# Optimization experiments

Measured on AMD Instinct MI355X. Metric: run time of the kernel, lower is better.

Reference implementation:

```python
import jax, jax.numpy as jnp
import numpy as np

EPS_BN = 1e-5
EPS_NORM = 1e-12
USER_NUM, ITEM_NUM = 100000, 50000
N_NODES = USER_NUM + ITEM_NUM
N_EDGES = 2400000
OUT_DIM, HID_DIM = 64, 128
BATCH = 4096


def setup_inputs() -> dict:
    key = jax.random.key(0)
    ks = jax.random.split(key, 12)
    f32 = jnp.float32
    return {
        "user_emb": jax.random.normal(ks[0], (USER_NUM, OUT_DIM), f32) * 0.1,
        "item_emb": jax.random.normal(ks[1], (ITEM_NUM, OUT_DIM), f32) * 0.1,
        "W0": jax.random.normal(ks[2], (OUT_DIM, HID_DIM), f32) * (1.0 / np.sqrt(OUT_DIM)),
        "b0": jnp.zeros((HID_DIM,), f32),
        "g0": jnp.ones((HID_DIM,), f32),
        "beta0": jnp.zeros((HID_DIM,), f32),
        "W1": jax.random.normal(ks[3], (HID_DIM, HID_DIM), f32) * (1.0 / np.sqrt(HID_DIM)),
        "b1": jnp.zeros((HID_DIM,), f32),
        "g1": jnp.ones((HID_DIM,), f32),
        "beta1": jnp.zeros((HID_DIM,), f32),
        "W2": jax.random.normal(ks[4], (HID_DIM, OUT_DIM), f32) * (1.0 / np.sqrt(HID_DIM)),
        "b2": jnp.zeros((OUT_DIM,), f32),
        "user_id": jax.random.randint(ks[5], (BATCH,), 0, USER_NUM),
        "pos_item": jax.random.randint(ks[6], (BATCH,), 0, ITEM_NUM),
        "neg_item": jax.random.randint(ks[7], (BATCH,), 0, ITEM_NUM),
        "edge_index": jax.random.randint(ks[8], (2, N_EDGES), 0, N_NODES),
    }


def _gcn_conv(x, W, b, src, dst, dis):
    # GCNConv with self-loops and symmetric normalization:
    # out_i = sum_{j->i} d_j^{-1/2} d_i^{-1/2} (x_j W) + d_i^{-1} (x_i W) + b
    h = x @ W                                   # [N, F]
    norm = dis[src] * dis[dst]                  # [E]
    msgs = h[src] * norm[:, None]               # [E, F] (irregular gather)
    agg = jax.ops.segment_sum(msgs, dst, num_segments=x.shape[0])
    self_loop = h * (dis * dis)[:, None]        # contribution of added self-loops
    return agg + self_loop + b


def _bn_train(x, gamma, beta):
    mean = jnp.mean(x, axis=0)
    var = jnp.mean((x - mean) ** 2, axis=0)     # biased var, as torch BN uses
    return (x - mean) * jax.lax.rsqrt(var + EPS_BN) * gamma + beta


def _l2norm(x):
    n = jnp.sqrt(jnp.sum(x * x, axis=-1, keepdims=True))
    return x / jnp.maximum(n, EPS_NORM)


def reference(user_emb, item_emb, W0, b0, g0, beta0, W1, b1, g1, beta1, W2, b2,
              user_id, pos_item, neg_item, edge_index):
    N = user_emb.shape[0] + item_emb.shape[0]
    src, dst = edge_index[0], edge_index[1]
    # degree includes self loop (weight 1 per edge + 1 self loop)
    deg = 1.0 + jax.ops.segment_sum(jnp.ones_like(src, user_emb.dtype), dst, num_segments=N)
    dis = jax.lax.rsqrt(deg)

    x = jnp.concatenate([user_emb, item_emb], axis=0)          # [N, OUT_DIM]

    # layer 0: conv -> BN -> ReLU -> (dropout: eval/identity) -> L2-normalize
    x = _l2norm(jax.nn.relu(_bn_train(_gcn_conv(x, W0, b0, src, dst, dis), g0, beta0)))
    # layer 1
    x = _l2norm(jax.nn.relu(_bn_train(_gcn_conv(x, W1, b1, src, dst, dis), g1, beta1)))
    # final conv
    x = _gcn_conv(x, W2, b2, src, dst, dis)                    # [N, OUT_DIM]

    user_embeddings = x[:user_emb.shape[0]]
    item_embeddings = x[user_emb.shape[0]:]
    u = user_embeddings[user_id]
    p = item_embeddings[pos_item]
    n = item_embeddings[neg_item]
    pos_score = jnp.sum(u * p, axis=-1)
    neg_score = jnp.sum(u * n, axis=-1)
    rec_loss = -jnp.mean(jax.nn.log_sigmoid(pos_score - neg_score))
    return rec_loss, x
```

## Files before the change

kernel.cpp:

```cpp
#include <hip/hip_runtime.h>
#include <hip/hip_bf16.h>
#include <math.h>

#define USER_NUM 100000
#define ITEM_NUM 50000
#define N_NODES  150000
#define N_EDGES  2400000
#define OUT_DIM  64
#define HID_DIM  128
#define BATCH    4096
#define EPS_BN   1e-5f

typedef unsigned short ushort_t;
typedef unsigned int uint_t;

__device__ __forceinline__ ushort_t f2bf(float f) {
    uint_t u = __float_as_uint(f);
    u += 0x7FFFu + ((u >> 16) & 1u);
    return (ushort_t)(u >> 16);
}
__device__ __forceinline__ float bf2f(ushort_t s) {
    return __uint_as_float((uint_t)s << 16);
}


__global__ __launch_bounds__(256) void zero_int_kernel(int* __restrict__ p, int n) {
    int i = blockIdx.x * 256 + threadIdx.x;
    if (i < n) p[i] = 0;
}

__global__ __launch_bounds__(256) void count_kernel(const int* __restrict__ dst, int* __restrict__ cnt) {
    int i = blockIdx.x * 256 + threadIdx.x;
    if (i < N_EDGES) atomicAdd(&cnt[dst[i]], 1);
}

__global__ __launch_bounds__(256) void dis_kernel(const int* __restrict__ cnt, float* __restrict__ dis) {
    int i = blockIdx.x * 256 + threadIdx.x;
    if (i < N_NODES) dis[i] = rsqrtf(1.0f + (float)cnt[i]);
}

#define SC_ELEM 1024
#define SC_NB   ((N_NODES + SC_ELEM - 1) / SC_ELEM)

__global__ __launch_bounds__(256) void scan_part_kernel(const int* __restrict__ cnt,
                                                        int* __restrict__ psum) {
    __shared__ int red[4];
    int tid = threadIdx.x;
    int base = blockIdx.x * SC_ELEM + tid * 4;
    int s = 0;
#pragma unroll
    for (int j = 0; j < 4; j++) { int i = base + j; if (i < N_NODES) s += cnt[i]; }
#pragma unroll
    for (int d = 1; d < 64; d <<= 1) s += __shfl_xor(s, d);
    if ((tid & 63) == 0) red[tid >> 6] = s;
    __syncthreads();
    if (tid == 0) psum[blockIdx.x] = red[0] + red[1] + red[2] + red[3];
}

__global__ __launch_bounds__(256) void scan_mid_kernel(int* __restrict__ psum,
                                                       int* __restrict__ off, int nb) {
    __shared__ int lds[256];
    int tid = threadIdx.x;
    int v = (tid < nb) ? psum[tid] : 0;
    lds[tid] = v;
    __syncthreads();
    for (int d = 1; d < 256; d <<= 1) {
        int t = (tid >= d) ? lds[tid - d] : 0;
        __syncthreads();
        lds[tid] += t;
        __syncthreads();
    }
    if (tid < nb) psum[tid] = lds[tid] - v;
    if (tid == 0) off[N_NODES] = lds[255];
}

__global__ __launch_bounds__(256) void scan_emit_kernel(const int* __restrict__ cnt,
                                                        const int* __restrict__ psum,
                                                        int* __restrict__ off) {
    __shared__ int lds[256];
    int tid = threadIdx.x;
    int base = blockIdx.x * SC_ELEM + tid * 4;
    int v[4]; int s = 0;
#pragma unroll
    for (int j = 0; j < 4; j++) {
        int i = base + j;
        v[j] = (i < N_NODES) ? cnt[i] : 0;
        s += v[j];
    }
    lds[tid] = s;
    __syncthreads();
    for (int d = 1; d < 256; d <<= 1) {
        int t = (tid >= d) ? lds[tid - d] : 0;
        __syncthreads();
        lds[tid] += t;
        __syncthreads();
    }
    int run = psum[blockIdx.x] + lds[tid] - s;
#pragma unroll
    for (int j = 0; j < 4; j++) {
        int i = base + j;
        if (i < N_NODES) off[i] = run;
        run += v[j];
    }
}


#define BSH   9
#define NBUCK ((N_NODES + 511) / 512)
#define P1_BLOCKS 512

__global__ __launch_bounds__(256) void bucket_part_kernel(const int* __restrict__ src,
                                                          const int* __restrict__ dst,
                                                          const int* __restrict__ off,
                                                          int* __restrict__ bcur,
                                                          uint2* __restrict__ temp) {
    __shared__ int hist[NBUCK];
    __shared__ int base[NBUCK];
    const int per = (N_EDGES + P1_BLOCKS - 1) / P1_BLOCKS;
    const int lo = blockIdx.x * per;
    int hi = lo + per; if (hi > N_EDGES) hi = N_EDGES;
    const int tid = threadIdx.x;
    for (int j = tid; j < NBUCK; j += 256) hist[j] = 0;
    __syncthreads();
    for (int i = lo + tid; i < hi; i += 256)
        atomicAdd(&hist[dst[i] >> BSH], 1);
    __syncthreads();
    for (int b = tid; b < NBUCK; b += 256) {
        int h = hist[b];
        if (h > 0) base[b] = off[b << BSH] + atomicAdd(&bcur[b], h);
    }
    __syncthreads();
    for (int i = lo + tid; i < hi; i += 256) {
        int d = dst[i];
        int p = atomicAdd(&base[d >> BSH], 1);
        temp[p] = make_uint2((uint_t)src[i], (uint_t)d);
    }
}

__global__ __launch_bounds__(256) void bucket_fine_kernel(const int* __restrict__ off,
                                                          const float* __restrict__ dis,
                                                          const uint2* __restrict__ temp,
                                                          uint2* __restrict__ csr8) {
    __shared__ int   offs[513];
    __shared__ int   cur[512];
    __shared__ float disd[512];
    const int b  = blockIdx.x;
    const int lo = b << BSH;
    int hi = lo + 512; if (hi > N_NODES) hi = N_NODES;
    const int nn = hi - lo;
    const int tid = threadIdx.x;
    for (int j = tid; j <= nn; j += 256) offs[j] = off[lo + j];
    for (int j = tid; j < nn; j += 256) { cur[j] = 0; disd[j] = dis[lo + j]; }
    __syncthreads();
    const int e0 = offs[0], e1 = offs[nn];
    for (int i = e0 + tid; i < e1; i += 256) {
        uint2 t = temp[i];
        int dl = (int)t.y - lo;
        int p = offs[dl] + atomicAdd(&cur[dl], 1);
        float wv = dis[t.x] * disd[dl];
        csr8[p] = make_uint2(t.x, __float_as_uint(wv));
    }
}


__device__ __forceinline__ float4 load4(const float* p) { return *(const float4*)p; }
__device__ __forceinline__ float4 load4(const ushort_t* p) {
    ushort4 u = *(const ushort4*)p;
    return make_float4(bf2f(u.x), bf2f(u.y), bf2f(u.z), bf2f(u.w));
}

template<typename XT, int DIN, int DOUT, int MBLK>
__global__ __launch_bounds__(256) void gemm_kernel(const XT* __restrict__ xlo,
                                                   const XT* __restrict__ xhi, int split,
                                                   const float* __restrict__ W,
                                                   ushort_t* __restrict__ out, int nrows) {
    constexpr int KC    = 32;
    constexpr int NC    = DIN / KC;
    constexpr int XS_PT = MBLK / 32;
    constexpr int WS_PT = DOUT / 32;
    constexpr int NCOLG = DOUT / 8;

    __shared__ float xs[MBLK][KC + 1];
    __shared__ float ws[KC][DOUT];

    const int tid  = threadIdx.x;
    const int row0 = blockIdx.x * MBLK;
    const int colg = tid % NCOLG;
    const int rowg = tid / NCOLG;

    float4 xr[XS_PT], wr[WS_PT];

    auto load_chunk = [&](int kc) {
#pragma unroll
        for (int i = 0; i < XS_PT; i++) {
            int idx = i * 256 + tid;
            int m = idx >> 3, kq = idx & 7;
            int row = row0 + m; if (row > nrows - 1) row = nrows - 1;
            const XT* rp = (row < split) ? xlo + (size_t)row * DIN
                                         : xhi + (size_t)(row - split) * DIN;
            xr[i] = load4(rp + kc + kq * 4);
        }
#pragma unroll
        for (int i = 0; i < WS_PT; i++) {
            int idx = i * 256 + tid;
            int n4 = idx % (DOUT / 4), kk = idx / (DOUT / 4);
            wr[i] = *(const float4*)(W + (size_t)(kc + kk) * DOUT + n4 * 4);
        }
    };
    auto write_chunk = [&]() {
#pragma unroll
        for (int i = 0; i < XS_PT; i++) {
            int idx = i * 256 + tid;
            int m = idx >> 3, kq = idx & 7;
            xs[m][kq * 4 + 0] = xr[i].x;
            xs[m][kq * 4 + 1] = xr[i].y;
            xs[m][kq * 4 + 2] = xr[i].z;
            xs[m][kq * 4 + 3] = xr[i].w;
        }
#pragma unroll
        for (int i = 0; i < WS_PT; i++) {
            int idx = i * 256 + tid;
            int n4 = idx % (DOUT / 4), kk = idx / (DOUT / 4);
            *(float4*)&ws[kk][n4 * 4] = wr[i];
        }
    };

    float acc[8][8];
#pragma unroll
    for (int r = 0; r < 8; r++)
#pragma unroll
        for (int c = 0; c < 8; c++) acc[r][c] = 0.f;

    load_chunk(0);
    write_chunk();
    __syncthreads();

    for (int c = 0; c < NC; c++) {
        if (c + 1 < NC) load_chunk((c + 1) * KC);
#pragma unroll 4
        for (int k = 0; k < KC; k++) {
            float4 wa = *(const float4*)&ws[k][colg * 8];
            float4 wb = *(const float4*)&ws[k][colg * 8 + 4];
            float xv[8];
#pragma unroll
            for (int r = 0; r < 8; r++) xv[r] = xs[rowg * 8 + r][k];
#pragma unroll
            for (int r = 0; r < 8; r++) {
                acc[r][0] = fmaf(xv[r], wa.x, acc[r][0]);
                acc[r][1] = fmaf(xv[r], wa.y, acc[r][1]);
                acc[r][2] = fmaf(xv[r], wa.z, acc[r][2]);
                acc[r][3] = fmaf(xv[r], wa.w, acc[r][3]);
                acc[r][4] = fmaf(xv[r], wb.x, acc[r][4]);
                acc[r][5] = fmaf(xv[r], wb.y, acc[r][5]);
                acc[r][6] = fmaf(xv[r], wb.z, acc[r][6]);
                acc[r][7] = fmaf(xv[r], wb.w, acc[r][7]);
            }
        }
        __syncthreads();
        if (c + 1 < NC) { write_chunk(); __syncthreads(); }
    }

#pragma unroll
    for (int r = 0; r < 8; r++) {
        int row = row0 + rowg * 8 + r;
        if (row < nrows) {
            uint4 pk;
            pk.x = (uint_t)f2bf(acc[r][0]) | ((uint_t)f2bf(acc[r][1]) << 16);
            pk.y = (uint_t)f2bf(acc[r][2]) | ((uint_t)f2bf(acc[r][3]) << 16);
            pk.z = (uint_t)f2bf(acc[r][4]) | ((uint_t)f2bf(acc[r][5]) << 16);
            pk.w = (uint_t)f2bf(acc[r][6]) | ((uint_t)f2bf(acc[r][7]) << 16);
            *(uint4*)&out[(size_t)row * DOUT + colg * 8] = pk;
        }
    }
}


template<int DOUT>
__global__ __launch_bounds__(256) void agg_kernel(const ushort_t* __restrict__ h,
                                                  const float* __restrict__ dis,
                                                  const int* __restrict__ off,
                                                  const uint2* __restrict__ csr8,
                                                  const float* __restrict__ bias,
                                                  float* __restrict__ out, int n) {
    int wave = threadIdx.x >> 6;
    int lane = threadIdx.x & 63;
    int node = blockIdx.x * 4 + wave;
    if (node >= n) return;
    float di  = dis[node];
    int   beg = off[node], end = off[node + 1];
    if (DOUT == 128) {
        const uint_t* hp = (const uint_t*)h;
        float ax = 0.f, ay = 0.f;
        int e = beg;
        for (; e + 4 <= end; e += 4) {
            uint2 e0 = csr8[e], e1 = csr8[e + 1], e2 = csr8[e + 2], e3 = csr8[e + 3];
            uint_t u0 = hp[(size_t)e0.x * 64 + lane];
            uint_t u1 = hp[(size_t)e1.x * 64 + lane];
            uint_t u2 = hp[(size_t)e2.x * 64 + lane];
            uint_t u3 = hp[(size_t)e3.x * 64 + lane];
            float w0 = __uint_as_float(e0.y), w1 = __uint_as_float(e1.y);
            float w2 = __uint_as_float(e2.y), w3 = __uint_as_float(e3.y);
            ax = fmaf(__uint_as_float(u0 << 16), w0, ax);
            ay = fmaf(__uint_as_float(u0 & 0xFFFF0000u), w0, ay);
            ax = fmaf(__uint_as_float(u1 << 16), w1, ax);
            ay = fmaf(__uint_as_float(u1 & 0xFFFF0000u), w1, ay);
            ax = fmaf(__uint_as_float(u2 << 16), w2, ax);
            ay = fmaf(__uint_as_float(u2 & 0xFFFF0000u), w2, ay);
            ax = fmaf(__uint_as_float(u3 << 16), w3, ax);
            ay = fmaf(__uint_as_float(u3 & 0xFFFF0000u), w3, ay);
        }
        for (; e < end; e++) {
            uint2 ev = csr8[e];
            float wv = __uint_as_float(ev.y);
            uint_t u = hp[(size_t)ev.x * 64 + lane];
            ax = fmaf(__uint_as_float(u << 16), wv, ax);
            ay = fmaf(__uint_as_float(u & 0xFFFF0000u), wv, ay);
        }
        uint_t us = hp[(size_t)node * 64 + lane];
        float2 bb = ((const float2*)bias)[lane];
        float dd = di * di;
        float2 o;
        o.x = ax + __uint_as_float(us << 16) * dd + bb.x;
        o.y = ay + __uint_as_float(us & 0xFFFF0000u) * dd + bb.y;
        ((float2*)out)[(size_t)node * 64 + lane] = o;
    } else {
        float ax = 0.f;
        int e = beg;
        for (; e + 4 <= end; e += 4) {
            uint2 e0 = csr8[e], e1 = csr8[e + 1], e2 = csr8[e + 2], e3 = csr8[e + 3];
            float h0 = bf2f(h[(size_t)e0.x * 64 + lane]);
            float h1 = bf2f(h[(size_t)e1.x * 64 + lane]);
            float h2 = bf2f(h[(size_t)e2.x * 64 + lane]);
            float h3 = bf2f(h[(size_t)e3.x * 64 + lane]);
            ax = fmaf(h0, __uint_as_float(e0.y), ax);
            ax = fmaf(h1, __uint_as_float(e1.y), ax);
            ax = fmaf(h2, __uint_as_float(e2.y), ax);
            ax = fmaf(h3, __uint_as_float(e3.y), ax);
        }
        for (; e < end; e++) {
            uint2 ev = csr8[e];
            ax = fmaf(bf2f(h[(size_t)ev.x * 64 + lane]), __uint_as_float(ev.y), ax);
        }
        float hs = bf2f(h[(size_t)node * 64 + lane]);
        out[(size_t)node * 64 + lane] = ax + hs * di * di + bias[lane];
    }
}


#define STATS_NB 512

__global__ __launch_bounds__(128) void stats1_kernel(const float* __restrict__ x,
                                                     double* __restrict__ part) {
    int col = threadIdx.x;
    double a = 0.0, b = 0.0;
    for (int row = blockIdx.x; row < N_NODES; row += STATS_NB) {
        float v = x[(size_t)row * HID_DIM + col];
        a += v;
        b += (double)v * (double)v;
    }
    part[(size_t)blockIdx.x * 256 + col]       = a;
    part[(size_t)blockIdx.x * 256 + 128 + col] = b;
}

__global__ __launch_bounds__(256) void stats2_kernel(const double* __restrict__ part,
                                                     const float* __restrict__ g,
                                                     const float* __restrict__ beta,
                                                     float* __restrict__ a_out,
                                                     float* __restrict__ b_out) {
    __shared__ double red1[4], red2[4];
    int col = blockIdx.x;
    int tid = threadIdx.x;
    double s1 = 0.0, s2 = 0.0;
    for (int p = tid; p < STATS_NB; p += 256) {
        s1 += part[(size_t)p * 256 + col];
        s2 += part[(size_t)p * 256 + 128 + col];
    }
#pragma unroll
    for (int d = 32; d >= 1; d >>= 1) {
        s1 += __shfl_xor(s1, d);
        s2 += __shfl_xor(s2, d);
    }
    int wave = tid >> 6, lane = tid & 63;
    if (lane == 0) { red1[wave] = s1; red2[wave] = s2; }
    __syncthreads();
    if (tid == 0) {
        double t1 = red1[0] + red1[1] + red1[2] + red1[3];
        double t2 = red2[0] + red2[1] + red2[2] + red2[3];
        double mean = t1 / (double)N_NODES;
        double var  = t2 / (double)N_NODES - mean * mean;
        float inv = rsqrtf((float)var + EPS_BN);
        float aa  = g[col] * inv;
        a_out[col] = aa;
        b_out[col] = beta[col] - (float)mean * aa;
    }
}


__global__ __launch_bounds__(256) void bn_relu_l2_kernel(const float* __restrict__ in,
                                                         const float* __restrict__ a,
                                                         const float* __restrict__ b,
                                                         uint_t* __restrict__ outp, int n) {
    int wave = threadIdx.x >> 6;
    int lane = threadIdx.x & 63;
    int row  = blockIdx.x * 4 + wave;
    if (row >= n) return;
    float2 v  = *(const float2*)(in + (size_t)row * 128 + lane * 2);
    float2 aa = *(const float2*)(a + lane * 2);
    float2 bb = *(const float2*)(b + lane * 2);
    float y0 = fmaxf(fmaf(v.x, aa.x, bb.x), 0.f);
    float y1 = fmaxf(fmaf(v.y, aa.y, bb.y), 0.f);
    float ss = y0 * y0 + y1 * y1;
#pragma unroll
    for (int d = 32; d >= 1; d >>= 1) ss += __shfl_xor(ss, d);
    float nn  = sqrtf(ss);
    float inv = 1.f / fmaxf(nn, 1e-12f);
    uint_t pk = (uint_t)f2bf(y0 * inv) | ((uint_t)f2bf(y1 * inv) << 16);
    outp[(size_t)row * 64 + lane] = pk;
}


__global__ void zero_float_kernel(float* p) { *p = 0.f; }

__global__ __launch_bounds__(256) void loss_kernel(const float* __restrict__ X,
                                                   const int* __restrict__ uid,
                                                   const int* __restrict__ pid,
                                                   const int* __restrict__ nid,
                                                   float* __restrict__ out0) {
    int wave = threadIdx.x >> 6;
    int lane = threadIdx.x & 63;
    int b = blockIdx.x * 4 + wave;
    if (b >= BATCH) return;
    const float* u = X + (size_t)uid[b] * OUT_DIM;
    const float* p = X + (size_t)(USER_NUM + pid[b]) * OUT_DIM;
    const float* q = X + (size_t)(USER_NUM + nid[b]) * OUT_DIM;
    float uv = u[lane];
    float ps = uv * p[lane];
    float ns = uv * q[lane];
#pragma unroll
    for (int d = 32; d >= 1; d >>= 1) {
        ps += __shfl_xor(ps, d);
        ns += __shfl_xor(ns, d);
    }
    if (lane == 0) {
        float t  = ns - ps;
        float sp = fmaxf(t, 0.f) + log1pf(expf(-fabsf(t)));
        atomicAdd(out0, sp * (1.0f / BATCH));
    }
}


extern "C" void kernel_launch(void* const* d_in, const int* in_sizes, int n_in,
                              void* d_out, int out_size, void* d_ws, size_t ws_size,
                              hipStream_t stream) {
    const float* user_emb = (const float*)d_in[0];
    const float* item_emb = (const float*)d_in[1];
    const float* W0  = (const float*)d_in[2];
    const float* b0  = (const float*)d_in[3];
    const float* g0  = (const float*)d_in[4];
    const float* be0 = (const float*)d_in[5];
    const float* W1  = (const float*)d_in[6];
    const float* b1  = (const float*)d_in[7];
    const float* g1  = (const float*)d_in[8];
    const float* be1 = (const float*)d_in[9];
    const float* W2  = (const float*)d_in[10];
    const float* b2  = (const float*)d_in[11];
    const int* user_id  = (const int*)d_in[12];
    const int* pos_item = (const int*)d_in[13];
    const int* neg_item = (const int*)d_in[14];
    const int* edge     = (const int*)d_in[15];
    const int* src = edge;
    const int* dst = edge + N_EDGES;

    char* w = (char*)d_ws;
    auto alloc = [&](size_t bytes) -> char* {
        char* r = w;
        w += (bytes + 255) / 256 * 256;
        return r;
    };
    int*      cnt  = (int*)alloc((size_t)N_NODES * 4);
    int*      off  = (int*)alloc((size_t)(N_NODES + 1) * 4);
    int*      bcur = (int*)alloc((size_t)NBUCK * 4);
    uint2*    csr8 = (uint2*)alloc((size_t)N_EDGES * 8);
    float*    dis  = (float*)alloc((size_t)N_NODES * 4);
    int*      psum = (int*)alloc((size_t)SC_NB * 4);
    double*   part = (double*)alloc((size_t)STATS_NB * 256 * 8);
    float*    bn_a = (float*)alloc(128 * 4);
    float*    bn_b = (float*)alloc(128 * 4);
    ushort_t* hbuf = (ushort_t*)alloc((size_t)N_NODES * HID_DIM * 2);
    float*    xbuf = (float*)alloc((size_t)N_NODES * HID_DIM * 4);
    ushort_t* xbf  = (ushort_t*)alloc((size_t)N_NODES * HID_DIM * 2);

    uint2* temp = (uint2*)hbuf;

    float* out = (float*)d_out;
    float* X   = out + 1;

    const int EB = (N_EDGES + 255) / 256;
    const int NB = (N_NODES + 255) / 256;
    const int AGGB = (N_NODES + 3) / 4;

    zero_int_kernel<<<NB, 256, 0, stream>>>(cnt, N_NODES);
    count_kernel<<<EB, 256, 0, stream>>>(dst, cnt);
    dis_kernel<<<NB, 256, 0, stream>>>(cnt, dis);
    scan_part_kernel<<<SC_NB, 256, 0, stream>>>(cnt, psum);
    scan_mid_kernel<<<1, 256, 0, stream>>>(psum, off, SC_NB);
    scan_emit_kernel<<<SC_NB, 256, 0, stream>>>(cnt, psum, off);
    zero_int_kernel<<<(NBUCK + 255) / 256, 256, 0, stream>>>(bcur, NBUCK);
    bucket_part_kernel<<<P1_BLOCKS, 256, 0, stream>>>(src, dst, off, bcur, temp);
    bucket_fine_kernel<<<NBUCK, 256, 0, stream>>>(off, dis, temp, csr8);

    gemm_kernel<float, 64, 128, 128><<<(N_NODES + 127) / 128, 256, 0, stream>>>(
        user_emb, item_emb, USER_NUM, W0, hbuf, N_NODES);
    agg_kernel<128><<<AGGB, 256, 0, stream>>>(hbuf, dis, off, csr8, b0, xbuf, N_NODES);
    stats1_kernel<<<STATS_NB, 128, 0, stream>>>(xbuf, part);
    stats2_kernel<<<128, 256, 0, stream>>>(part, g0, be0, bn_a, bn_b);
    bn_relu_l2_kernel<<<AGGB, 256, 0, stream>>>(xbuf, bn_a, bn_b, (uint_t*)xbf, N_NODES);

    gemm_kernel<ushort_t, 128, 128, 128><<<(N_NODES + 127) / 128, 256, 0, stream>>>(
        xbf, xbf, N_NODES, W1, hbuf, N_NODES);
    agg_kernel<128><<<AGGB, 256, 0, stream>>>(hbuf, dis, off, csr8, b1, xbuf, N_NODES);
    stats1_kernel<<<STATS_NB, 128, 0, stream>>>(xbuf, part);
    stats2_kernel<<<128, 256, 0, stream>>>(part, g1, be1, bn_a, bn_b);
    bn_relu_l2_kernel<<<AGGB, 256, 0, stream>>>(xbuf, bn_a, bn_b, (uint_t*)xbf, N_NODES);

    gemm_kernel<ushort_t, 128, 64, 256><<<(N_NODES + 255) / 256, 256, 0, stream>>>(
        xbf, xbf, N_NODES, W2, hbuf, N_NODES);
    agg_kernel<64><<<AGGB, 256, 0, stream>>>(hbuf, dis, off, csr8, b2, X, N_NODES);

    zero_float_kernel<<<1, 1, 0, stream>>>(out);
    loss_kernel<<<(BATCH + 3) / 4, 256, 0, stream>>>(X, user_id, pos_item, neg_item, out);
}
```

Measured before the change: 1.077 ms.

## Rewrite node-feature GEMM to use bf16 MFMA matrix instructions

Replaces the FP32 FMA shared-memory tiled GEMM with a kernel that uses 16x16x32 bf16 MFMA instructions. The weights are converted to bf16 and held transposed in LDS, and each wave computes 32 rows directly from global loads. This targets the dense projection cost in each GCN layer. In exchange, weights and the first-layer embeddings are rounded to bf16, and output stores become narrow 2-byte scattered writes.

Measured after the change: 967.5 us. 1.11x faster.

```diff
diff --git a/kernel.cpp b/kernel.cpp
--- a/kernel.cpp
+++ b/kernel.cpp
@@ -13,6 +13,9 @@
 
 typedef unsigned short ushort_t;
 typedef unsigned int uint_t;
+
+typedef __attribute__((ext_vector_type(8))) __bf16 bf16x8;
+typedef __attribute__((ext_vector_type(4))) float f32x4;
 
 __device__ __forceinline__ ushort_t f2bf(float f) {
     uint_t u = __float_as_uint(f);
@@ -163,113 +166,78 @@
 }
 
 
-__device__ __forceinline__ float4 load4(const float* p) { return *(const float4*)p; }
-__device__ __forceinline__ float4 load4(const ushort_t* p) {
-    ushort4 u = *(const ushort4*)p;
-    return make_float4(bf2f(u.x), bf2f(u.y), bf2f(u.z), bf2f(u.w));
-}
-
-template<typename XT, int DIN, int DOUT, int MBLK>
+__device__ __forceinline__ bf16x8 loadA(const ushort_t* p) {
+    uint4 u = *(const uint4*)p;
+    return __builtin_bit_cast(bf16x8, u);
+}
+__device__ __forceinline__ bf16x8 loadA(const float* p) {
+    float4 f0 = *(const float4*)p;
+    float4 f1 = *(const float4*)(p + 4);
+    uint4 u;
+    u.x = (uint_t)f2bf(f0.x) | ((uint_t)f2bf(f0.y) << 16);
+    u.y = (uint_t)f2bf(f0.z) | ((uint_t)f2bf(f0.w) << 16);
+    u.z = (uint_t)f2bf(f1.x) | ((uint_t)f2bf(f1.y) << 16);
+    u.w = (uint_t)f2bf(f1.z) | ((uint_t)f2bf(f1.w) << 16);
+    return __builtin_bit_cast(bf16x8, u);
+}
+
+template<typename XT, int DIN, int DOUT>
 __global__ __launch_bounds__(256) void gemm_kernel(const XT* __restrict__ xlo,
                                                    const XT* __restrict__ xhi, int split,
                                                    const float* __restrict__ W,
                                                    ushort_t* __restrict__ out, int nrows) {
-    constexpr int KC    = 32;
-    constexpr int NC    = DIN / KC;
-    constexpr int XS_PT = MBLK / 32;
-    constexpr int WS_PT = DOUT / 32;
-    constexpr int NCOLG = DOUT / 8;
-
-    __shared__ float xs[MBLK][KC + 1];
-    __shared__ float ws[KC][DOUT];
-
-    const int tid  = threadIdx.x;
-    const int row0 = blockIdx.x * MBLK;
-    const int colg = tid % NCOLG;
-    const int rowg = tid / NCOLG;
-
-    float4 xr[XS_PT], wr[WS_PT];
-
-    auto load_chunk = [&](int kc) {
-#pragma unroll
-        for (int i = 0; i < XS_PT; i++) {
-            int idx = i * 256 + tid;
-            int m = idx >> 3, kq = idx & 7;
-            int row = row0 + m; if (row > nrows - 1) row = nrows - 1;
-            const XT* rp = (row < split) ? xlo + (size_t)row * DIN
-                                         : xhi + (size_t)(row - split) * DIN;
-            xr[i] = load4(rp + kc + kq * 4);
+    constexpr int LDW = DIN + 8;
+    constexpr int NCT = DOUT / 16;
+    __shared__ ushort_t wt[DOUT][LDW];
+
+    const int tid = threadIdx.x;
+    for (int idx = tid; idx < DIN * DOUT; idx += 256) {
+        int k = idx / DOUT, n = idx % DOUT;
+        wt[n][k] = f2bf(W[idx]);
+    }
+    __syncthreads();
+
+    const int wave = tid >> 6, lane = tid & 63;
+    const int lm = lane & 15, lk = lane >> 4;
+    const int row0 = blockIdx.x * 128 + wave * 32;
+
+    f32x4 acc[2][NCT];
+#pragma unroll
+    for (int rt = 0; rt < 2; rt++)
+#pragma unroll
+        for (int c = 0; c < NCT; c++) acc[rt][c] = (f32x4){0.f, 0.f, 0.f, 0.f};
+
+    const XT* rp[2];
+#pragma unroll
+    for (int rt = 0; rt < 2; rt++) {
+        int row = row0 + rt * 16 + lm;
+        if (row > nrows - 1) row = nrows - 1;
+        rp[rt] = (row < split) ? xlo + (size_t)row * DIN
+                               : xhi + (size_t)(row - split) * DIN;
+    }
+
+#pragma unroll
+    for (int ks = 0; ks < DIN / 32; ks++) {
+        bf16x8 a0 = loadA(rp[0] + ks * 32 + lk * 8);
+        bf16x8 a1 = loadA(rp[1] + ks * 32 + lk * 8);
+#pragma unroll
+        for (int c = 0; c < NCT; c++) {
+            bf16x8 b = *(const bf16x8*)&wt[c * 16 + lm][ks * 32 + lk * 8];
+            acc[0][c] = __builtin_amdgcn_mfma_f32_16x16x32_bf16(a0, b, acc[0][c], 0, 0, 0);
+            acc[1][c] = __builtin_amdgcn_mfma_f32_16x16x32_bf16(a1, b, acc[1][c], 0, 0, 0);
         }
-#pragma unroll
-        for (int i = 0; i < WS_PT; i++) {
-            int idx = i * 256 + tid;
-            int n4 = idx % (DOUT / 4), kk = idx / (DOUT / 4);
-            wr[i] = *(const float4*)(W + (size_t)(kc + kk) * DOUT + n4 * 4);
-        }
-    };
-    auto write_chunk = [&]() {
-#pragma unroll
-        for (int i = 0; i < XS_PT; i++) {
-            int idx = i * 256 + tid;
-            int m = idx >> 3, kq = idx & 7;
-            xs[m][kq * 4 + 0] = xr[i].x;
-            xs[m][kq * 4 + 1] = xr[i].y;
-            xs[m][kq * 4 + 2] = xr[i].z;
-            xs[m][kq * 4 + 3] = xr[i].w;
-        }
-#pragma unroll
-        for (int i = 0; i < WS_PT; i++) {
-            int idx = i * 256 + tid;
-            int n4 = idx % (DOUT / 4), kk = idx / (DOUT / 4);
-            *(float4*)&ws[kk][n4 * 4] = wr[i];
-        }
-    };
-
-    float acc[8][8];
-#pragma unroll
-    for (int r = 0; r < 8; r++)
-#pragma unroll
-        for (int c = 0; c < 8; c++) acc[r][c] = 0.f;
-
-    load_chunk(0);
-    write_chunk();
-    __syncthreads();
-
-    for (int c = 0; c < NC; c++) {
-        if (c + 1 < NC) load_chunk((c + 1) * KC);
-#pragma unroll 4
-        for (int k = 0; k < KC; k++) {
-            float4 wa = *(const float4*)&ws[k][colg * 8];
-            float4 wb = *(const float4*)&ws[k][colg * 8 + 4];
-            float xv[8];
-#pragma unroll
-            for (int r = 0; r < 8; r++) xv[r] = xs[rowg * 8 + r][k];
-#pragma unroll
-            for (int r = 0; r < 8; r++) {
-                acc[r][0] = fmaf(xv[r], wa.x, acc[r][0]);
-                acc[r][1] = fmaf(xv[r], wa.y, acc[r][1]);
-                acc[r][2] = fmaf(xv[r], wa.z, acc[r][2]);
-                acc[r][3] = fmaf(xv[r], wa.w, acc[r][3]);
-                acc[r][4] = fmaf(xv[r], wb.x, acc[r][4]);
-                acc[r][5] = fmaf(xv[r], wb.y, acc[r][5]);
-                acc[r][6] = fmaf(xv[r], wb.z, acc[r][6]);
-                acc[r][7] = fmaf(xv[r], wb.w, acc[r][7]);
+    }
+
+#pragma unroll
+    for (int rt = 0; rt < 2; rt++) {
+#pragma unroll
+        for (int r = 0; r < 4; r++) {
+            int row = row0 + rt * 16 + lk * 4 + r;
+            if (row < nrows) {
+#pragma unroll
+                for (int c = 0; c < NCT; c++)
+                    out[(size_t)row * DOUT + c * 16 + lm] = f2bf(acc[rt][c][r]);
             }
-        }
-        __syncthreads();
-        if (c + 1 < NC) { write_chunk(); __syncthreads(); }
-    }
-
-#pragma unroll
-    for (int r = 0; r < 8; r++) {
-        int row = row0 + rowg * 8 + r;
-        if (row < nrows) {
-            uint4 pk;
-            pk.x = (uint_t)f2bf(acc[r][0]) | ((uint_t)f2bf(acc[r][1]) << 16);
-            pk.y = (uint_t)f2bf(acc[r][2]) | ((uint_t)f2bf(acc[r][3]) << 16);
-            pk.z = (uint_t)f2bf(acc[r][4]) | ((uint_t)f2bf(acc[r][5]) << 16);
-            pk.w = (uint_t)f2bf(acc[r][6]) | ((uint_t)f2bf(acc[r][7]) << 16);
-            *(uint4*)&out[(size_t)row * DOUT + colg * 8] = pk;
         }
     }
 }
@@ -498,6 +466,7 @@
     const int EB = (N_EDGES + 255) / 256;
     const int NB = (N_NODES + 255) / 256;
     const int AGGB = (N_NODES + 3) / 4;
+    const int GB = (N_NODES + 127) / 128;
 
     zero_int_kernel<<<NB, 256, 0, stream>>>(cnt, N_NODES);
     count_kernel<<<EB, 256, 0, stream>>>(dst, cnt);
@@ -509,21 +478,21 @@
     bucket_part_kernel<<<P1_BLOCKS, 256, 0, stream>>>(src, dst, off, bcur, temp);
     bucket_fine_kernel<<<NBUCK, 256, 0, stream>>>(off, dis, temp, csr8);
 
-    gemm_kernel<float, 64, 128, 128><<<(N_NODES + 127) / 128, 256, 0, stream>>>(
+    gemm_kernel<float, 64, 128><<<GB, 256, 0, stream>>>(
         user_emb, item_emb, USER_NUM, W0, hbuf, N_NODES);
     agg_kernel<128><<<AGGB, 256, 0, stream>>>(hbuf, dis, off, csr8, b0, xbuf, N_NODES);
     stats1_kernel<<<STATS_NB, 128, 0, stream>>>(xbuf, part);
     stats2_kernel<<<128, 256, 0, stream>>>(part, g0, be0, bn_a, bn_b);
     bn_relu_l2_kernel<<<AGGB, 256, 0, stream>>>(xbuf, bn_a, bn_b, (uint_t*)xbf, N_NODES);
 
-    gemm_kernel<ushort_t, 128, 128, 128><<<(N_NODES + 127) / 128, 256, 0, stream>>>(
+    gemm_kernel<ushort_t, 128, 128><<<GB, 256, 0, stream>>>(
         xbf, xbf, N_NODES, W1, hbuf, N_NODES);
     agg_kernel<128><<<AGGB, 256, 0, stream>>>(hbuf, dis, off, csr8, b1, xbuf, N_NODES);
     stats1_kernel<<<STATS_NB, 128, 0, stream>>>(xbuf, part);
     stats2_kernel<<<128, 256, 0, stream>>>(part, g1, be1, bn_a, bn_b);
     bn_relu_l2_kernel<<<AGGB, 256, 0, stream>>>(xbuf, bn_a, bn_b, (uint_t*)xbf, N_NODES);
 
-    gemm_kernel<ushort_t, 128, 64, 256><<<(N_NODES + 255) / 256, 256, 0, stream>>>(
+    gemm_kernel<ushort_t, 128, 64><<<GB, 256, 0, stream>>>(
         xbf, xbf, N_NODES, W2, hbuf, N_NODES);
     agg_kernel<64><<<AGGB, 256, 0, stream>>>(hbuf, dis, off, csr8, b2, X, N_NODES);
 
```
